# Performance work log

Measured on AMD Instinct MI355X. Metric: run time of the kernel, lower is better.

## Reference

```python
import jax, jax.numpy as jnp
import numpy as np

N_NODES = 50000
N_EDGES = 800000
N_GRAPHS = 512
VOCAB = 128
HID = 64
NCLS = 5


def _seg_mean(vals, ids, num_segments):
    s = jax.ops.segment_sum(vals, ids, num_segments=num_segments)
    cnt = jax.ops.segment_sum(jnp.ones((vals.shape[0],), vals.dtype), ids, num_segments=num_segments)
    return s / jnp.maximum(cnt, 1.0)[:, None]


def sage_conv(x, src, dst, W_l, b_l, W_r):
    # PyG SAGEConv (mean aggr): out = lin_l(mean_{j in N(i)} x_j) + lin_r(x_i)
    agg = _seg_mean(x[src], dst, x.shape[0])          # [N, H] gather + scatter-mean
    return agg @ W_l.T + b_l + x @ W_r.T


def setup_inputs() -> dict:
    key = jax.random.key(0)
    ks = jax.random.split(key, 10)
    scale = 1.0 / np.sqrt(HID)
    x_tokens = jax.random.randint(ks[0], (N_NODES,), 0, VOCAB)
    edge_index = jax.random.randint(ks[1], (2, N_EDGES), 0, N_NODES)
    batch = jnp.sort(jax.random.randint(ks[2], (N_NODES,), 0, N_GRAPHS))
    return {
        "x_tokens": x_tokens,
        "edge_index": edge_index,
        "batch": batch,
        "embed": jax.random.normal(ks[3], (VOCAB, HID), jnp.float32),
        "W1l": jax.random.normal(ks[4], (HID, HID), jnp.float32) * scale,
        "b1l": jnp.zeros((HID,), jnp.float32),
        "W1r": jax.random.normal(ks[5], (HID, HID), jnp.float32) * scale,
        "W2l": jax.random.normal(ks[6], (HID, HID), jnp.float32) * scale,
        "b2l": jnp.zeros((HID,), jnp.float32),
        "W2r": jax.random.normal(ks[7], (HID, HID), jnp.float32) * scale,
        "Wlin": jax.random.normal(ks[8], (NCLS, HID), jnp.float32) * scale,
        "blin": jnp.zeros((NCLS,), jnp.float32),
    }


def reference(x_tokens, edge_index, batch, embed, W1l, b1l, W1r, W2l, b2l, W2r, Wlin, blin):
    src, dst = edge_index[0], edge_index[1]
    x = embed[x_tokens]                                  # [N, H] embedding lookup
    x = jax.nn.relu(sage_conv(x, src, dst, W1l, b1l, W1r))
    x = jax.nn.relu(sage_conv(x, src, dst, W2l, b2l, W2r))
    g = _seg_mean(x, batch, N_GRAPHS)                    # global_mean_pool -> [G, H]
    return g @ Wlin.T + blin                             # [G, num_classes]
```

## Files before the change

kernel.cpp:

```cpp
#include <hip/hip_runtime.h>

#define N_NODES  50000
#define N_EDGES  800000
#define N_GRAPHS 512
#define HID      64
#define NCLS     5
#define NB       64
#define EST      36
#define AST      68

typedef __attribute__((ext_vector_type(8))) short bf16x8;
typedef __attribute__((ext_vector_type(4))) float f32x4;

__device__ inline unsigned short f2bf(float f) {
    unsigned int u = __builtin_bit_cast(unsigned int, f);
    unsigned int r = (u + 0x7FFFu + ((u >> 16) & 1u)) >> 16;
    return (unsigned short)r;
}
__device__ inline unsigned int packbf(float a, float b) {
    return (unsigned int)f2bf(a) | ((unsigned int)f2bf(b) << 16);
}
__device__ inline float bf2f(unsigned int u16) {
    unsigned int t = u16 << 16;
    return __builtin_bit_cast(float, t);
}

#define XCDS   8
#define NPX    (N_NODES / XCDS)
#define EPB    512
#define ECH2   ((N_EDGES + EPB - 1) / EPB)
#define SEC_E  (ECH2 * XCDS * 256)
#define EBUF_T (128 * 32)
#define PW_T   (64 * 64)
#define PREP_T (SEC_E + EBUF_T + N_NODES + 2 * PW_T)
__global__ void k_prep_fill(
    const int* __restrict__ src, const int* __restrict__ dst,
    const int* __restrict__ tok,
    int* __restrict__ cnt, unsigned int* __restrict__ bucket,
    const float* __restrict__ embed, unsigned int* __restrict__ ebufg,
    const int* __restrict__ batch,
    int* __restrict__ pos_start, int* __restrict__ pos_end,
    const float* __restrict__ W1l, const float* __restrict__ W1r,
    unsigned int* __restrict__ wb1,
    const float* __restrict__ W2l, const float* __restrict__ W2r,
    unsigned int* __restrict__ wb2) {
    int gid = blockIdx.x * blockDim.x + threadIdx.x;
    if (gid < SEC_E) {
        int blk   = gid >> 8;
        int tidl  = gid & 255;
        int range = blk & 7;
        int chunk = blk >> 3;
        int lo = range * NPX;
        int e0 = chunk * EPB + tidl;
        int e1 = e0 + 256;
        int d0 = (e0 < N_EDGES) ? dst[e0] : -1;
        int d1 = (e1 < N_EDGES) ? dst[e1] : -1;
        int s0 = (e0 < N_EDGES) ? src[e0] : 0;
        int s1 = (e1 < N_EDGES) ? src[e1] : 0;
        bool k0 = (d0 >= lo) && (d0 < lo + NPX);
        bool k1 = (d1 >= lo) && (d1 < lo + NPX);
        unsigned int t0 = k0 ? (unsigned int)tok[s0] : 0u;
        unsigned int t1 = k1 ? (unsigned int)tok[s1] : 0u;
        if (k0) {
            int pos = atomicAdd(&cnt[d0], 1);
            if (pos < NB) bucket[(long)d0 * NB + pos] = (unsigned int)s0 | (t0 << 16);
        }
        if (k1) {
            int pos = atomicAdd(&cnt[d1], 1);
            if (pos < NB) bucket[(long)d1 * NB + pos] = (unsigned int)s1 | (t1 << 16);
        }
        return;
    }
    gid -= SEC_E;
    if (gid < EBUF_T) {
        int t = gid >> 5, c = gid & 31;
        float2 v = ((const float2*)(embed + (long)t * HID))[c];
        ebufg[gid] = packbf(v.x, v.y);
        return;
    }
    gid -= EBUF_T;
    if (gid < N_NODES) {
        int n = gid;
        int b = batch[n];
        if (n == 0 || batch[n - 1] != b) pos_start[b] = n;
        if (n == N_NODES - 1 || batch[n + 1] != b) pos_end[b] = n + 1;
        return;
    }
    gid -= N_NODES;
    if (gid < 2 * PW_T) {
        const float* Wl = (gid < PW_T) ? W1l : W2l;
        const float* Wr = (gid < PW_T) ? W1r : W2r;
        unsigned int* wb = (gid < PW_T) ? wb1 : wb2;
        int i = (gid < PW_T) ? gid : gid - PW_T;
        int h = i >> 6, c = i & 63;
        float2 v = (c < 32) ? ((const float2*)(Wl + (long)h * HID))[c]
                            : ((const float2*)(Wr + (long)h * HID))[c - 32];
        wb[i] = packbf(v.x, v.y);
    }
}

template <bool L1, int NPBT>
__global__ __launch_bounds__(NPBT * 16) void k_layer(
    const int* __restrict__ cnt, const unsigned int* __restrict__ bucket,
    const int* __restrict__ tok, const unsigned int* __restrict__ ebufg,
    const unsigned int* __restrict__ xb,
    const unsigned int* __restrict__ wb, const float* __restrict__ bl,
    unsigned short* __restrict__ xoutb)
{
    __shared__ unsigned int As[NPBT * AST];
    __shared__ unsigned int elds[L1 ? 128 * EST : 1];
    const int tid  = threadIdx.x;
    const int wv   = tid >> 6;
    const int lane = tid & 63;
    const int n0   = blockIdx.x * NPBT;

    if (L1) {
        for (int i = tid; i < EBUF_T; i += NPBT * 16) {
            int t = i >> 5, c = i & 31;
            elds[t * EST + c] = ebufg[i];
        }
        __syncthreads();
    }

    const int q  = lane & 7;
    const int e8 = lane >> 3;

#pragma unroll
    for (int i = 0; i < 4; ++i) {
        int rl = wv * 4 + i;
        int nn = n0 + rl;
        int nc = min(nn, N_NODES - 1);
        int deg = cnt[nc];
        int m   = (nn < N_NODES) ? min(deg, NB) : 0;
        unsigned int v = (lane < m) ? bucket[(long)nc * NB + lane] : 0u;
        float f0 = 0, f1 = 0, f2 = 0, f3 = 0, f4 = 0, f5 = 0, f6 = 0, f7 = 0;
#pragma unroll
        for (int g = 0; g < 8; ++g) {
            int j = g * 8 + e8;
            unsigned int vv = __shfl(v, j, 64);
            if (j < m) {
                uint4 w4;
                if (L1) w4 = *(const uint4*)(elds + (vv >> 16) * EST + q * 4);
                else    w4 = *((const uint4*)(xb + (long)(vv & 0xffffu) * 32) + q);
                f0 += bf2f(w4.x & 0xffff); f1 += bf2f(w4.x >> 16);
                f2 += bf2f(w4.y & 0xffff); f3 += bf2f(w4.y >> 16);
                f4 += bf2f(w4.z & 0xffff); f5 += bf2f(w4.z >> 16);
                f6 += bf2f(w4.w & 0xffff); f7 += bf2f(w4.w >> 16);
            }
        }
#pragma unroll
        for (int o = 8; o < 64; o <<= 1) {
            f0 += __shfl_xor(f0, o, 64); f1 += __shfl_xor(f1, o, 64);
            f2 += __shfl_xor(f2, o, 64); f3 += __shfl_xor(f3, o, 64);
            f4 += __shfl_xor(f4, o, 64); f5 += __shfl_xor(f5, o, 64);
            f6 += __shfl_xor(f6, o, 64); f7 += __shfl_xor(f7, o, 64);
        }
        if (e8 == 0) {
            float inv = 1.0f / (float)max(deg, 1);
            uint4 o;
            o.x = packbf(f0 * inv, f1 * inv);
            o.y = packbf(f2 * inv, f3 * inv);
            o.z = packbf(f4 * inv, f5 * inv);
            o.w = packbf(f6 * inv, f7 * inv);
            *(uint4*)(As + rl * AST + q * 4) = o;
        } else if (e8 == 1) {
            uint4 sv;
            if (L1) { int tk = tok[nc]; sv = *(const uint4*)(elds + tk * EST + q * 4); }
            else    { sv = *((const uint4*)(xb + (long)nc * 32) + q); }
            *(uint4*)(As + rl * AST + 32 + q * 4) = sv;
        }
    }
    __syncthreads();

    constexpr int NSTR = NPBT / 16;
    const int s    = wv % NSTR;
    const int t    = wv / NSTR;
    const int mm   = lane & 15;
    const int quad = lane >> 4;

    bf16x8 afr[4];
#pragma unroll
    for (int kst = 0; kst < 4; ++kst)
        afr[kst] = *(const bf16x8*)(As + (s * 16 + mm) * AST + kst * 16 + quad * 4);

    f32x4 acc = (f32x4){0.f, 0.f, 0.f, 0.f};
#pragma unroll
    for (int kst = 0; kst < 4; ++kst) {
        bf16x8 bfr = *(const bf16x8*)(wb + (t * 16 + mm) * 64 + kst * 16 + quad * 4);
        acc = __builtin_amdgcn_mfma_f32_16x16x32_bf16(bfr, afr[kst], acc, 0, 0, 0);
    }

    int node = n0 + s * 16 + mm;
    if (node < N_NODES) {
        int hb = t * 16 + quad * 4;
        float4 bb = *(const float4*)(bl + hb);
        ushort4 o;
        o.x = f2bf(fmaxf(acc[0] + bb.x, 0.f));
        o.y = f2bf(fmaxf(acc[1] + bb.y, 0.f));
        o.z = f2bf(fmaxf(acc[2] + bb.z, 0.f));
        o.w = f2bf(fmaxf(acc[3] + bb.w, 0.f));
        *(ushort4*)(xoutb + (long)node * HID + hb) = o;
    }
}

__global__ __launch_bounds__(256) void k_pool(
    const unsigned int* __restrict__ x2b,
    const int* __restrict__ pos_start, const int* __restrict__ pos_end,
    const float* __restrict__ Wlin, const float* __restrict__ blin,
    float* __restrict__ out)
{
    __shared__ float part[4][8][8];
    int g    = blockIdx.x;
    int tid  = threadIdx.x;
    int wv   = tid >> 6;
    int lane = tid & 63;
    int q    = lane & 7;
    int slot = wv * 8 + (lane >> 3);
    int s = pos_start[g], e = pos_end[g];
    float f0 = 0, f1 = 0, f2 = 0, f3 = 0, f4 = 0, f5 = 0, f6 = 0, f7 = 0;
    for (int n = s + slot; n < e; n += 32) {
        uint4 v = *((const uint4*)(x2b + (long)n * 32) + q);
        f0 += bf2f(v.x & 0xffff); f1 += bf2f(v.x >> 16);
        f2 += bf2f(v.y & 0xffff); f3 += bf2f(v.y >> 16);
        f4 += bf2f(v.z & 0xffff); f5 += bf2f(v.z >> 16);
        f6 += bf2f(v.w & 0xffff); f7 += bf2f(v.w >> 16);
    }
#pragma unroll
    for (int o = 8; o < 64; o <<= 1) {
        f0 += __shfl_xor(f0, o, 64); f1 += __shfl_xor(f1, o, 64);
        f2 += __shfl_xor(f2, o, 64); f3 += __shfl_xor(f3, o, 64);
        f4 += __shfl_xor(f4, o, 64); f5 += __shfl_xor(f5, o, 64);
        f6 += __shfl_xor(f6, o, 64); f7 += __shfl_xor(f7, o, 64);
    }
    if (lane < 8) {
        part[wv][lane][0] = f0; part[wv][lane][1] = f1;
        part[wv][lane][2] = f2; part[wv][lane][3] = f3;
        part[wv][lane][4] = f4; part[wv][lane][5] = f5;
        part[wv][lane][6] = f6; part[wv][lane][7] = f7;
    }
    __syncthreads();
    if (wv == 0) {
        f0 = part[0][q][0] + part[1][q][0] + part[2][q][0] + part[3][q][0];
        f1 = part[0][q][1] + part[1][q][1] + part[2][q][1] + part[3][q][1];
        f2 = part[0][q][2] + part[1][q][2] + part[2][q][2] + part[3][q][2];
        f3 = part[0][q][3] + part[1][q][3] + part[2][q][3] + part[3][q][3];
        f4 = part[0][q][4] + part[1][q][4] + part[2][q][4] + part[3][q][4];
        f5 = part[0][q][5] + part[1][q][5] + part[2][q][5] + part[3][q][5];
        f6 = part[0][q][6] + part[1][q][6] + part[2][q][6] + part[3][q][6];
        f7 = part[0][q][7] + part[1][q][7] + part[2][q][7] + part[3][q][7];
        float inv = 1.0f / (float)max(e - s, 1);
        f0 *= inv; f1 *= inv; f2 *= inv; f3 *= inv;
        f4 *= inv; f5 *= inv; f6 *= inv; f7 *= inv;
#pragma unroll
        for (int c = 0; c < NCLS; ++c) {
            const float* wr = Wlin + c * HID + q * 8;
            float p = f0 * wr[0] + f1 * wr[1] + f2 * wr[2] + f3 * wr[3] +
                      f4 * wr[4] + f5 * wr[5] + f6 * wr[6] + f7 * wr[7];
            p += __shfl_xor(p, 1, 64);
            p += __shfl_xor(p, 2, 64);
            p += __shfl_xor(p, 4, 64);
            if (lane == 0) out[g * NCLS + c] = p + blin[c];
        }
    }
}

extern "C" void kernel_launch(void* const* d_in, const int* in_sizes, int n_in,
                              void* d_out, int out_size, void* d_ws, size_t ws_size,
                              hipStream_t stream) {
    const int*   tok   = (const int*)d_in[0];
    const int*   eidx  = (const int*)d_in[1];
    const int*   batch = (const int*)d_in[2];
    const float* embed = (const float*)d_in[3];
    const float* W1l   = (const float*)d_in[4];
    const float* b1l   = (const float*)d_in[5];
    const float* W1r   = (const float*)d_in[6];
    const float* W2l   = (const float*)d_in[7];
    const float* b2l   = (const float*)d_in[8];
    const float* W2r   = (const float*)d_in[9];
    const float* Wlin  = (const float*)d_in[10];
    const float* blin  = (const float*)d_in[11];
    float* out = (float*)d_out;

    const int* src = eidx;
    const int* dst = eidx + N_EDGES;

    char* wsp = (char*)d_ws;
    size_t off = 0;
    auto alloc = [&](size_t bytes) -> void* {
        void* p = wsp + off;
        off = (off + bytes + 255) & ~(size_t)255;
        return p;
    };
    int*   cnt     = (int*)  alloc((size_t)N_NODES * 4);
    int*   pstart  = (int*)  alloc((size_t)N_GRAPHS * 4);
    int*   pend    = (int*)  alloc((size_t)N_GRAPHS * 4);
    unsigned int* bucket = (unsigned int*)alloc((size_t)N_NODES * NB * 4);
    unsigned int* x1b    = (unsigned int*)alloc((size_t)N_NODES * 32 * 4);
    unsigned int* x2b    = (unsigned int*)alloc((size_t)N_NODES * 32 * 4);
    unsigned int* ebufg  = (unsigned int*)alloc((size_t)128 * 32 * 4);
    unsigned int* wb1    = (unsigned int*)alloc((size_t)64 * 64 * 4);
    unsigned int* wb2    = (unsigned int*)alloc((size_t)64 * 64 * 4);

    hipMemsetAsync(cnt, 0, (char*)pend - (char*)cnt + (size_t)N_GRAPHS * 4, stream);

    k_prep_fill<<<(PREP_T + 255) / 256, 256, 0, stream>>>(
        src, dst, tok, cnt, bucket,
        embed, ebufg, batch, pstart, pend, W1l, W1r, wb1, W2l, W2r, wb2);

    k_layer<true, 32><<<(N_NODES + 31) / 32, 512, 0, stream>>>(
        cnt, bucket, tok, ebufg, nullptr, wb1, b1l, (unsigned short*)x1b);
    k_layer<false, 16><<<(N_NODES + 15) / 16, 256, 0, stream>>>(
        cnt, bucket, nullptr, nullptr, x1b, wb2, b2l, (unsigned short*)x2b);

    k_pool<<<N_GRAPHS, 256, 0, stream>>>(x2b, pstart, pend, Wlin, blin, out);
}
```

Before: 188.1 us.

## Fuse global mean pool and classifier into layer-2 kernel via atomics

```diff
diff --git a/kernel.cpp b/kernel.cpp
--- a/kernel.cpp
+++ b/kernel.cpp
@@ -105,10 +105,16 @@
     const int* __restrict__ tok, const unsigned int* __restrict__ ebufg,
     const unsigned int* __restrict__ xb,
     const unsigned int* __restrict__ wb, const float* __restrict__ bl,
-    unsigned short* __restrict__ xoutb)
+    unsigned short* __restrict__ xoutb,
+    const int* __restrict__ batch, float* __restrict__ gacc,
+    int* __restrict__ done,
+    const int* __restrict__ pstart, const int* __restrict__ pend,
+    const float* __restrict__ Wlin, const float* __restrict__ blin,
+    float* __restrict__ out)
 {
     __shared__ unsigned int As[NPBT * AST];
     __shared__ unsigned int elds[L1 ? 128 * EST : 1];
+    __shared__ int s_last;
     const int tid  = threadIdx.x;
     const int wv   = tid >> 6;
     const int lane = tid & 63;
@@ -191,75 +197,59 @@
     }
 
     int node = n0 + s * 16 + mm;
-    if (node < N_NODES) {
-        int hb = t * 16 + quad * 4;
-        float4 bb = *(const float4*)(bl + hb);
-        ushort4 o;
-        o.x = f2bf(fmaxf(acc[0] + bb.x, 0.f));
-        o.y = f2bf(fmaxf(acc[1] + bb.y, 0.f));
-        o.z = f2bf(fmaxf(acc[2] + bb.z, 0.f));
-        o.w = f2bf(fmaxf(acc[3] + bb.w, 0.f));
-        *(ushort4*)(xoutb + (long)node * HID + hb) = o;
-    }
-}
-
-__global__ __launch_bounds__(256) void k_pool(
-    const unsigned int* __restrict__ x2b,
-    const int* __restrict__ pos_start, const int* __restrict__ pos_end,
-    const float* __restrict__ Wlin, const float* __restrict__ blin,
-    float* __restrict__ out)
-{
-    __shared__ float part[4][8][8];
-    int g    = blockIdx.x;
-    int tid  = threadIdx.x;
-    int wv   = tid >> 6;
-    int lane = tid & 63;
-    int q    = lane & 7;
-    int slot = wv * 8 + (lane >> 3);
-    int s = pos_start[g], e = pos_end[g];
-    float f0 = 0, f1 = 0, f2 = 0, f3 = 0, f4 = 0, f5 = 0, f6 = 0, f7 = 0;
-    for (int n = s + slot; n < e; n += 32) {
-        uint4 v = *((const uint4*)(x2b + (long)n * 32) + q);
-        f0 += bf2f(v.x & 0xffff); f1 += bf2f(v.x >> 16);
-        f2 += bf2f(v.y & 0xffff); f3 += bf2f(v.y >> 16);
-        f4 += bf2f(v.z & 0xffff); f5 += bf2f(v.z >> 16);
-        f6 += bf2f(v.w & 0xffff); f7 += bf2f(v.w >> 16);
-    }
-#pragma unroll
-    for (int o = 8; o < 64; o <<= 1) {
-        f0 += __shfl_xor(f0, o, 64); f1 += __shfl_xor(f1, o, 64);
-        f2 += __shfl_xor(f2, o, 64); f3 += __shfl_xor(f3, o, 64);
-        f4 += __shfl_xor(f4, o, 64); f5 += __shfl_xor(f5, o, 64);
-        f6 += __shfl_xor(f6, o, 64); f7 += __shfl_xor(f7, o, 64);
-    }
-    if (lane < 8) {
-        part[wv][lane][0] = f0; part[wv][lane][1] = f1;
-        part[wv][lane][2] = f2; part[wv][lane][3] = f3;
-        part[wv][lane][4] = f4; part[wv][lane][5] = f5;
-        part[wv][lane][6] = f6; part[wv][lane][7] = f7;
-    }
-    __syncthreads();
-    if (wv == 0) {
-        f0 = part[0][q][0] + part[1][q][0] + part[2][q][0] + part[3][q][0];
-        f1 = part[0][q][1] + part[1][q][1] + part[2][q][1] + part[3][q][1];
-        f2 = part[0][q][2] + part[1][q][2] + part[2][q][2] + part[3][q][2];
-        f3 = part[0][q][3] + part[1][q][3] + part[2][q][3] + part[3][q][3];
-        f4 = part[0][q][4] + part[1][q][4] + part[2][q][4] + part[3][q][4];
-        f5 = part[0][q][5] + part[1][q][5] + part[2][q][5] + part[3][q][5];
-        f6 = part[0][q][6] + part[1][q][6] + part[2][q][6] + part[3][q][6];
-        f7 = part[0][q][7] + part[1][q][7] + part[2][q][7] + part[3][q][7];
-        float inv = 1.0f / (float)max(e - s, 1);
-        f0 *= inv; f1 *= inv; f2 *= inv; f3 *= inv;
-        f4 *= inv; f5 *= inv; f6 *= inv; f7 *= inv;
-#pragma unroll
-        for (int c = 0; c < NCLS; ++c) {
-            const float* wr = Wlin + c * HID + q * 8;
-            float p = f0 * wr[0] + f1 * wr[1] + f2 * wr[2] + f3 * wr[3] +
-                      f4 * wr[4] + f5 * wr[5] + f6 * wr[6] + f7 * wr[7];
-            p += __shfl_xor(p, 1, 64);
-            p += __shfl_xor(p, 2, 64);
-            p += __shfl_xor(p, 4, 64);
-            if (lane == 0) out[g * NCLS + c] = p + blin[c];
+    int hb = t * 16 + quad * 4;
+    float4 bb = *(const float4*)(bl + hb);
+    float a0 = fmaxf(acc[0] + bb.x, 0.f);
+    float a1 = fmaxf(acc[1] + bb.y, 0.f);
+    float a2 = fmaxf(acc[2] + bb.z, 0.f);
+    float a3 = fmaxf(acc[3] + bb.w, 0.f);
+
+    if constexpr (L1) {
+        if (node < N_NODES) {
+            ushort4 o;
+            o.x = f2bf(a0); o.y = f2bf(a1); o.z = f2bf(a2); o.w = f2bf(a3);
+            *(ushort4*)(xoutb + (long)node * HID + hb) = o;
+        }
+    } else {
+        int g = batch[node];
+#pragma unroll
+        for (int off = 1; off < 16; off <<= 1) {
+            float o0 = __shfl_up(a0, off, 16), o1 = __shfl_up(a1, off, 16);
+            float o2 = __shfl_up(a2, off, 16), o3 = __shfl_up(a3, off, 16);
+            int   og = __shfl_up(g, off, 16);
+            if (mm >= off && og == g) { a0 += o0; a1 += o1; a2 += o2; a3 += o3; }
+        }
+        int gn = __shfl_down(g, 1, 16);
+        if (mm == 15 || gn != g) {
+            float* dp = gacc + g * HID + hb;
+            unsafeAtomicAdd(dp + 0, a0);
+            unsafeAtomicAdd(dp + 1, a1);
+            unsafeAtomicAdd(dp + 2, a2);
+            unsafeAtomicAdd(dp + 3, a3);
+        }
+        __threadfence();
+        __syncthreads();
+        if (tid == 0) s_last = (atomicAdd(done, 1) == (int)gridDim.x - 1);
+        __syncthreads();
+        if (s_last) {
+            for (int g2 = tid; g2 < N_GRAPHS; g2 += NPBT * 16) {
+                int c2 = pend[g2] - pstart[g2];
+                float inv = 1.0f / (float)max(c2, 1);
+                float s0 = 0, s1 = 0, s2 = 0, s3 = 0, s4 = 0;
+                for (int k = 0; k < HID; ++k) {
+                    float mk = unsafeAtomicAdd(gacc + g2 * HID + k, 0.0f) * inv;
+                    s0 += mk * Wlin[0 * HID + k];
+                    s1 += mk * Wlin[1 * HID + k];
+                    s2 += mk * Wlin[2 * HID + k];
+                    s3 += mk * Wlin[3 * HID + k];
+                    s4 += mk * Wlin[4 * HID + k];
+                }
+                out[g2 * NCLS + 0] = s0 + blin[0];
+                out[g2 * NCLS + 1] = s1 + blin[1];
+                out[g2 * NCLS + 2] = s2 + blin[2];
+                out[g2 * NCLS + 3] = s3 + blin[3];
+                out[g2 * NCLS + 4] = s4 + blin[4];
+            }
         }
     }
 }
@@ -294,23 +284,24 @@
     int*   cnt     = (int*)  alloc((size_t)N_NODES * 4);
     int*   pstart  = (int*)  alloc((size_t)N_GRAPHS * 4);
     int*   pend    = (int*)  alloc((size_t)N_GRAPHS * 4);
+    float* gacc    = (float*)alloc((size_t)N_GRAPHS * HID * 4);
+    int*   done    = (int*)  alloc(4);
     unsigned int* bucket = (unsigned int*)alloc((size_t)N_NODES * NB * 4);
     unsigned int* x1b    = (unsigned int*)alloc((size_t)N_NODES * 32 * 4);
-    unsigned int* x2b    = (unsigned int*)alloc((size_t)N_NODES * 32 * 4);
     unsigned int* ebufg  = (unsigned int*)alloc((size_t)128 * 32 * 4);
     unsigned int* wb1    = (unsigned int*)alloc((size_t)64 * 64 * 4);
     unsigned int* wb2    = (unsigned int*)alloc((size_t)64 * 64 * 4);
 
-    hipMemsetAsync(cnt, 0, (char*)pend - (char*)cnt + (size_t)N_GRAPHS * 4, stream);
+    hipMemsetAsync(cnt, 0, ((char*)done + 4) - (char*)cnt, stream);
 
     k_prep_fill<<<(PREP_T + 255) / 256, 256, 0, stream>>>(
         src, dst, tok, cnt, bucket,
         embed, ebufg, batch, pstart, pend, W1l, W1r, wb1, W2l, W2r, wb2);
 
     k_layer<true, 32><<<(N_NODES + 31) / 32, 512, 0, stream>>>(
-        cnt, bucket, tok, ebufg, nullptr, wb1, b1l, (unsigned short*)x1b);
-    k_layer<false, 16><<<(N_NODES + 15) / 16, 256, 0, stream>>>(
-        cnt, bucket, nullptr, nullptr, x1b, wb2, b2l, (unsigned short*)x2b);
-
-    k_pool<<<N_GRAPHS, 256, 0, stream>>>(x2b, pstart, pend, Wlin, blin, out);
-}
+        cnt, bucket, tok, ebufg, nullptr, wb1, b1l, (unsigned short*)x1b,
+        nullptr, nullptr, nullptr, nullptr, nullptr, nullptr, nullptr, nullptr);
+    k_layer<false, 16><<<N_NODES / 16, 256, 0, stream>>>(
+        cnt, bucket, nullptr, nullptr, x1b, wb2, b2l, nullptr,
+        batch, gacc, done, pstart, pend, Wlin, blin, out);
+}
```

New measurement: 470.3 us. +150.1%, slower.
